# Performance work log

Measured on AMD Instinct MI355X. Metric: run time of the kernel, lower is better.

Reference implementation:

```python
import jax, jax.numpy as jnp
import numpy as np

B, T, C, NH = 4, 2048, 1024, 16
HD = C // NH  # head dim = 64


def setup_inputs() -> dict:
    key = jax.random.key(0)
    k1, k2, k3 = jax.random.split(key, 3)
    x = jax.random.normal(k1, (B, T, C), dtype=jnp.float32)
    w_attn = jax.random.normal(k2, (C, 3 * C), dtype=jnp.float32) * (1.0 / np.sqrt(C))
    b_attn = jnp.zeros((3 * C,), dtype=jnp.float32)
    w_proj = jax.random.normal(k3, (C, C), dtype=jnp.float32) * (1.0 / np.sqrt(C))
    b_proj = jnp.zeros((C,), dtype=jnp.float32)
    return {"x": x, "w_attn": w_attn, "b_attn": b_attn, "w_proj": w_proj, "b_proj": b_proj}


def reference(x, w_attn, b_attn, w_proj, b_proj):
    Bx, Tx, Cx = x.shape
    # fused QKV projection
    qkv = x @ w_attn + b_attn              # [B, T, 3C]
    q, k, v = jnp.split(qkv, 3, axis=-1)   # each [B, T, C]
    # split heads: [B, NH, T, HD]
    q = q.reshape(Bx, Tx, NH, HD).transpose(0, 2, 1, 3)
    k = k.reshape(Bx, Tx, NH, HD).transpose(0, 2, 1, 3)
    v = v.reshape(Bx, Tx, NH, HD).transpose(0, 2, 1, 3)
    scale = 1.0 / np.sqrt(HD)
    att = jnp.einsum('bhqd,bhkd->bhqk', q, k) * scale  # [B, NH, T, T]
    causal = jnp.tril(jnp.ones((Tx, Tx), dtype=bool))
    att = jnp.where(causal[None, None], att, -jnp.inf)
    att = jax.nn.softmax(att, axis=-1)
    y = jnp.einsum('bhqk,bhkd->bhqd', att, v)           # [B, NH, T, HD]
    y = y.transpose(0, 2, 1, 3).reshape(Bx, Tx, Cx)
    return y @ w_proj + b_proj
```

## Files before the change

kernel.cpp:

```cpp
#include <hip/hip_runtime.h>
#include <hip/hip_bf16.h>

#define B_SZ 4
#define T_SZ 2048
#define C_SZ 1024
#define NH_SZ 16
#define HD_SZ 64
#define M_SZ (B_SZ * T_SZ)

typedef __bf16 bf16x8 __attribute__((ext_vector_type(8)));
typedef __bf16 bf16x4 __attribute__((ext_vector_type(4)));
typedef float f32x4 __attribute__((ext_vector_type(4)));

__device__ __forceinline__ void async_ld16(__hip_bfloat16* lds, const __hip_bfloat16* g) {
  __builtin_amdgcn_global_load_lds(
      (const __attribute__((address_space(1))) void*)g,
      (__attribute__((address_space(3))) void*)lds, 16, 0, 0);
}

__device__ __forceinline__ void bar() {
  asm volatile("" ::: "memory");
  __builtin_amdgcn_s_barrier();
  asm volatile("" ::: "memory");
}

__device__ __forceinline__ bf16x8 frag32(const __hip_bfloat16* base, int row, int q) {
  const int byte = (row << 6) + (((q ^ (row >> 1)) & 3) << 4);
  return *(const bf16x8*)((const char*)base + byte);
}

__device__ __forceinline__ uint32_t pk2(float lo, float hi) {
  uint32_t r;
  asm("v_cvt_pk_bf16_f32 %0, %1, %2" : "=v"(r) : "v"(lo), "v"(hi));
  return r;
}

__global__ __launch_bounds__(256) void conv_bf16_kernel(
    const float* __restrict__ X, __hip_bfloat16* __restrict__ Y) {
  const int i = (blockIdx.x * 256 + threadIdx.x) * 4;
  float4 v = *(const float4*)&X[i];
  union { bf16x4 v; __hip_bfloat16 h[4]; } o;
  o.h[0] = __float2bfloat16(v.x); o.h[1] = __float2bfloat16(v.y);
  o.h[2] = __float2bfloat16(v.z); o.h[3] = __float2bfloat16(v.w);
  *(bf16x4*)&Y[i] = o.v;
}

template <int KD, int ND>
__global__ __launch_bounds__(256) void transpose_conv_kernel(
    const float* __restrict__ W, __hip_bfloat16* __restrict__ Wt) {
  __shared__ float sT[32][33];
  const int n0 = blockIdx.x * 32, k0 = blockIdx.y * 32;
  const int tid = threadIdx.x;
  {
    const int r = tid >> 3, c = (tid & 7) * 4;
    float4 v = *(const float4*)&W[(size_t)(k0 + r) * ND + n0 + c];
    sT[r][c] = v.x; sT[r][c + 1] = v.y; sT[r][c + 2] = v.z; sT[r][c + 3] = v.w;
  }
  __syncthreads();
  {
    const int n = tid >> 3, kq = (tid & 7) * 4;
    union { bf16x4 v; __hip_bfloat16 h[4]; } o;
#pragma unroll
    for (int j = 0; j < 4; ++j) o.h[j] = __float2bfloat16(sT[kq + j][n]);
    *(bf16x4*)&Wt[(size_t)(n0 + n) * KD + k0 + kq] = o.v;
  }
}


#define Q_PRESCALE 0.18033688011112042f

__global__ __launch_bounds__(512, 2) void gemm_tri256_qk(
    const __hip_bfloat16* __restrict__ A, const __hip_bfloat16* __restrict__ Bt,
    const float* __restrict__ bias,
    __hip_bfloat16* __restrict__ qR, __hip_bfloat16* __restrict__ kR) {
  __shared__ __align__(16) __hip_bfloat16 sA[3][256 * 32];
  __shared__ __align__(16) __hip_bfloat16 sB[3][256 * 32];

  const int tid = threadIdx.x;
  const int wave = tid >> 6, lane = tid & 63;
  const int quad = lane >> 4, l16 = lane & 15;
  const int wm = wave >> 2, wn = wave & 3;

  const int xcd = (int)blockIdx.x & 7, lb = (int)blockIdx.x >> 3;
  const int bm = (xcd * 4 + (lb >> 3)) * 256;
  const int bn = (lb & 7) * 256;

  const int srow = tid >> 2;
  const int scol = 8 * ((tid & 3) ^ ((tid >> 3) & 3));
  const int sdst = tid * 8;
  const __hip_bfloat16* gA = A + (size_t)(bm + srow) * C_SZ + scol;
  const __hip_bfloat16* gB = Bt + (size_t)(bn + srow) * C_SZ + scol;

  f32x4 acc[8][4];
#pragma unroll
  for (int m = 0; m < 8; ++m)
#pragma unroll
    for (int n = 0; n < 4; ++n) acc[m][n] = (f32x4){0.f, 0.f, 0.f, 0.f};

#define STG256(buf, kt)                                                         \
  do {                                                                          \
    async_ld16(&sA[buf][sdst], gA + (kt) * 32);                                 \
    async_ld16(&sA[buf][4096 + sdst], gA + (size_t)128 * C_SZ + (kt) * 32);     \
    async_ld16(&sB[buf][sdst], gB + (kt) * 32);                                 \
    async_ld16(&sB[buf][4096 + sdst], gB + (size_t)128 * C_SZ + (kt) * 32);     \
  } while (0)

  STG256(0, 0);
  STG256(1, 1);
  asm volatile("s_waitcnt vmcnt(4)" ::: "memory");
  bar();

  constexpr int NT = C_SZ / 32;
  int cur = 0;
  for (int kt = 0; kt < NT; ++kt) {
    const int stg = cur == 0 ? 2 : cur - 1;
    if (kt + 2 < NT) STG256(stg, kt + 2);

    const __hip_bfloat16* ab = sA[cur];
    const __hip_bfloat16* bb = sB[cur];
    bf16x8 af[8], bfr[4];
#pragma unroll
    for (int mq = 0; mq < 8; ++mq) af[mq] = frag32(ab, wm * 128 + mq * 16 + l16, quad);
#pragma unroll
    for (int nq = 0; nq < 4; ++nq) bfr[nq] = frag32(bb, wn * 64 + nq * 16 + l16, quad);
#pragma unroll
    for (int mq = 0; mq < 8; ++mq)
#pragma unroll
      for (int nq = 0; nq < 4; ++nq)
        acc[mq][nq] = __builtin_amdgcn_mfma_f32_16x16x32_bf16(af[mq], bfr[nq], acc[mq][nq], 0, 0, 0);

    if (kt + 1 < NT) {
      if (kt + 2 < NT) asm volatile("s_waitcnt vmcnt(4)" ::: "memory");
      else             asm volatile("s_waitcnt vmcnt(0)" ::: "memory");
      bar();
    }
    cur = cur == 2 ? 0 : cur + 1;
  }
#undef STG256

  float bv[4];
#pragma unroll
  for (int nq = 0; nq < 4; ++nq) bv[nq] = bias[bn + wn * 64 + nq * 16 + l16];
  const bool isQ = bn < C_SZ;
#pragma unroll
  for (int mq = 0; mq < 8; ++mq)
#pragma unroll
    for (int nq = 0; nq < 4; ++nq) {
      const int col = bn + wn * 64 + nq * 16 + l16;
      const int hh = (col >> 6) & 15, d = col & 63;
#pragma unroll
      for (int r = 0; r < 4; ++r) {
        const int row = bm + wm * 128 + mq * 16 + quad * 4 + r;
        const int bb_ = row >> 11, t = row & 2047;
        const size_t idx = ((size_t)(bb_ * 16 + hh) * T_SZ + t) * HD_SZ + d;
        const float val = acc[mq][nq][r] + bv[nq];
        if (isQ) qR[idx] = __float2bfloat16(val * Q_PRESCALE);
        else     kR[idx] = __float2bfloat16(val);
      }
    }
}

template <int MODE>
__global__ __launch_bounds__(256, 3) void gemm_tri128(
    const __hip_bfloat16* __restrict__ A, const __hip_bfloat16* __restrict__ Bt,
    const float* __restrict__ bias, float* __restrict__ Cf,
    __hip_bfloat16* __restrict__ vT) {
  __shared__ __align__(16) __hip_bfloat16 sA[3][128 * 32];
  __shared__ __align__(16) __hip_bfloat16 sB[3][128 * 32];

  const int tid = threadIdx.x;
  const int wave = tid >> 6, lane = tid & 63;
  const int quad = lane >> 4, l16 = lane & 15;
  const int rw = (wave & 1) * 64, cw = (wave >> 1) * 64;

  const int xcd = (int)blockIdx.x & 7, lb = (int)blockIdx.x >> 3;
  const int bm = (xcd * 8 + (lb >> 3)) * 128;
  const int bn = (lb & 7) * 128;

  const int srow = tid >> 2;
  const int scol = 8 * ((tid & 3) ^ ((tid >> 3) & 3));
  const int sdst = tid * 8;
  const __hip_bfloat16* gA = A + (size_t)(bm + srow) * C_SZ + scol;
  const __hip_bfloat16* gB = Bt + (size_t)(bn + srow) * C_SZ + scol;

  f32x4 acc[4][4];
#pragma unroll
  for (int i = 0; i < 4; ++i)
#pragma unroll
    for (int j = 0; j < 4; ++j) acc[i][j] = (f32x4){0.f, 0.f, 0.f, 0.f};

#define STG128(buf, kt)                                                        \
  do {                                                                         \
    async_ld16(&sA[buf][sdst], gA + (kt) * 32);                                \
    async_ld16(&sA[buf][2048 + sdst], gA + (size_t)64 * C_SZ + (kt) * 32);     \
    async_ld16(&sB[buf][sdst], gB + (kt) * 32);                                \
    async_ld16(&sB[buf][2048 + sdst], gB + (size_t)64 * C_SZ + (kt) * 32);     \
  } while (0)

  STG128(0, 0);
  STG128(1, 1);
  asm volatile("s_waitcnt vmcnt(4)" ::: "memory");
  bar();

  constexpr int NT = C_SZ / 32;
  int cur = 0;
  for (int kt = 0; kt < NT; ++kt) {
    const int stg = cur == 0 ? 2 : cur - 1;
    if (kt + 2 < NT) STG128(stg, kt + 2);

    const __hip_bfloat16* ab = sA[cur];
    const __hip_bfloat16* bb = sB[cur];
    bf16x8 af[4], bfr[4];
#pragma unroll
    for (int mq = 0; mq < 4; ++mq) af[mq] = frag32(ab, rw + mq * 16 + l16, quad);
#pragma unroll
    for (int nq = 0; nq < 4; ++nq) bfr[nq] = frag32(bb, cw + nq * 16 + l16, quad);
#pragma unroll
    for (int mq = 0; mq < 4; ++mq)
#pragma unroll
      for (int nq = 0; nq < 4; ++nq)
        acc[mq][nq] = __builtin_amdgcn_mfma_f32_16x16x32_bf16(af[mq], bfr[nq], acc[mq][nq], 0, 0, 0);

    if (kt + 1 < NT) {
      if (kt + 2 < NT) asm volatile("s_waitcnt vmcnt(4)" ::: "memory");
      else             asm volatile("s_waitcnt vmcnt(0)" ::: "memory");
      bar();
    }
    cur = cur == 2 ? 0 : cur + 1;
  }
#undef STG128

  float bv[4];
#pragma unroll
  for (int nq = 0; nq < 4; ++nq) bv[nq] = bias[bn + cw + nq * 16 + l16];
#pragma unroll
  for (int mq = 0; mq < 4; ++mq)
#pragma unroll
    for (int nq = 0; nq < 4; ++nq) {
      const int col = bn + cw + nq * 16 + l16;
#pragma unroll
      for (int r = 0; r < 4; ++r) {
        const int row = bm + rw + mq * 16 + quad * 4 + r;
        const float val = acc[mq][nq][r] + bv[nq];
        if (MODE == 0) {
          const int bb_ = row >> 11, t = row & 2047;
          const int hh = col >> 6, d = col & 63;
          vT[((size_t)(bb_ * 16 + hh) * HD_SZ + d) * T_SZ + t] = __float2bfloat16(val);
        } else {
          Cf[(size_t)row * C_SZ + col] = val;
        }
      }
    }
}

#define ATT_ST 72

__global__ __launch_bounds__(256, 5) void attn_mfma_kernel(
    const __hip_bfloat16* __restrict__ qR, const __hip_bfloat16* __restrict__ kR,
    const __hip_bfloat16* __restrict__ vT, __hip_bfloat16* __restrict__ y) {
  __shared__ __align__(16) __hip_bfloat16 sQ[64][ATT_ST];
  __shared__ __align__(16) __hip_bfloat16 sK[64][ATT_ST];
  __shared__ __align__(16) __hip_bfloat16 sVt[64][ATT_ST];

  const int bh = blockIdx.x;
  const int tile = (int)gridDim.y - 1 - blockIdx.y;
  const int t0 = tile * 64;
  const int tid = threadIdx.x;
  const int wave = tid >> 6, lane = tid & 63;
  const int quad = lane >> 4, l16 = lane & 15;
  const int wrow0 = wave * 16;

  const __hip_bfloat16* qb = qR + (size_t)bh * T_SZ * HD_SZ;
  const __hip_bfloat16* kb = kR + (size_t)bh * T_SZ * HD_SZ;
  const __hip_bfloat16* vb = vT + (size_t)bh * HD_SZ * T_SZ;

  const int sr = tid >> 2, sc = (tid & 3) * 16;

  const bool uSel = (quad & 1) != 0;
  const bool cSel = (quad >> 1) != 0;
  const int srcE = l16 + 32 * (quad & 1) + 16 * (quad >> 1);
  const int srcO = srcE ^ 16;

  {
    const __hip_bfloat16* src = qb + (size_t)t0 * HD_SZ + tid * 16;
    *(float4*)&sQ[sr][sc] = *(const float4*)src;
    *(float4*)&sQ[sr][sc + 8] = *(const float4*)(src + 8);
  }

  float4 krg0, krg1, vrg0, vrg1;
  {
    const __hip_bfloat16* ks = kb + tid * 16;
    krg0 = *(const float4*)ks;
    krg1 = *(const float4*)(ks + 8);
    const __hip_bfloat16* vs = vb + (size_t)sr * T_SZ + sc;
    vrg0 = *(const float4*)vs;
    vrg1 = *(const float4*)(vs + 8);
  }

  __syncthreads();
  bf16x8 qa0 = *(const bf16x8*)&sQ[wrow0 + l16][quad * 8];
  bf16x8 qa1 = *(const bf16x8*)&sQ[wrow0 + l16][32 + quad * 8];

  float lacc = 0.f;
  f32x4 o[4];
#pragma unroll
  for (int nn = 0; nn < 4; ++nn) o[nn] = (f32x4){0.f, 0.f, 0.f, 0.f};

  for (int j0 = 0; j0 <= t0; j0 += 64) {
    *(float4*)&sK[sr][sc] = krg0;
    *(float4*)&sK[sr][sc + 8] = krg1;
    *(float4*)&sVt[sr][sc] = vrg0;
    *(float4*)&sVt[sr][sc + 8] = vrg1;
    if (j0 + 64 <= t0) {
      const __hip_bfloat16* ks = kb + (size_t)(j0 + 64) * HD_SZ + tid * 16;
      krg0 = *(const float4*)ks;
      krg1 = *(const float4*)(ks + 8);
      const __hip_bfloat16* vs = vb + (size_t)sr * T_SZ + j0 + 64 + sc;
      vrg0 = *(const float4*)vs;
      vrg1 = *(const float4*)(vs + 8);
    }
    __syncthreads();

    f32x4 s[4];
    __builtin_amdgcn_s_setprio(1);
#pragma unroll
    for (int sub = 0; sub < 4; ++sub) {
      s[sub] = (f32x4){0.f, 0.f, 0.f, 0.f};
      bf16x8 kf0 = *(const bf16x8*)&sK[sub * 16 + l16][quad * 8];
      s[sub] = __builtin_amdgcn_mfma_f32_16x16x32_bf16(kf0, qa0, s[sub], 0, 0, 0);
      bf16x8 kf1 = *(const bf16x8*)&sK[sub * 16 + l16][32 + quad * 8];
      s[sub] = __builtin_amdgcn_mfma_f32_16x16x32_bf16(kf1, qa1, s[sub], 0, 0, 0);
    }
    __builtin_amdgcn_s_setprio(0);

    if (j0 == t0) {
      const int qrow = wrow0 + l16;
#pragma unroll
      for (int sub = 0; sub < 4; ++sub)
#pragma unroll
        for (int r = 0; r < 4; ++r)
          if (sub * 16 + quad * 4 + r > qrow) s[sub][r] = -1e30f;
    }

#pragma unroll
    for (int sub = 0; sub < 4; ++sub)
#pragma unroll
      for (int r = 0; r < 4; ++r) s[sub][r] = __builtin_amdgcn_exp2f(s[sub][r]);
#pragma unroll
    for (int sub = 0; sub < 4; ++sub)
      lacc += (s[sub][0] + s[sub][1]) + (s[sub][2] + s[sub][3]);

    uint32_t pk[4][2];
#pragma unroll
    for (int sub = 0; sub < 4; ++sub)
#pragma unroll
      for (int h = 0; h < 2; ++h)
        pk[sub][h] = pk2(s[sub][2 * h], s[sub][2 * h + 1]);

    uint32_t g0 = (uint32_t)__shfl((int)(uSel ? pk[1][0] : pk[0][0]), srcE, 64);
    uint32_t g1 = (uint32_t)__shfl((int)(uSel ? pk[0][0] : pk[1][0]), srcO, 64);
    uint32_t g2 = (uint32_t)__shfl((int)(uSel ? pk[3][0] : pk[2][0]), srcE, 64);
    uint32_t g3 = (uint32_t)__shfl((int)(uSel ? pk[2][0] : pk[3][0]), srcO, 64);
    uint32_t g4 = (uint32_t)__shfl((int)(uSel ? pk[1][1] : pk[0][1]), srcE, 64);
    uint32_t g5 = (uint32_t)__shfl((int)(uSel ? pk[0][1] : pk[1][1]), srcO, 64);
    uint32_t g6 = (uint32_t)__shfl((int)(uSel ? pk[3][1] : pk[2][1]), srcE, 64);
    uint32_t g7 = (uint32_t)__shfl((int)(uSel ? pk[2][1] : pk[3][1]), srcO, 64);

    union PU { uint32_t d[4]; bf16x8 v; };
    PU A0, A1;
    A0.d[0] = cSel ? g1 : g0;  A0.d[1] = cSel ? g5 : g4;
    A0.d[2] = cSel ? g0 : g1;  A0.d[3] = cSel ? g4 : g5;
    A1.d[0] = cSel ? g3 : g2;  A1.d[1] = cSel ? g7 : g6;
    A1.d[2] = cSel ? g2 : g3;  A1.d[3] = cSel ? g6 : g7;

    __builtin_amdgcn_s_setprio(1);
#pragma unroll
    for (int nn = 0; nn < 4; ++nn) {
      bf16x8 vf0 = *(const bf16x8*)&sVt[nn * 16 + l16][quad * 8];
      o[nn] = __builtin_amdgcn_mfma_f32_16x16x32_bf16(A0.v, vf0, o[nn], 0, 0, 0);
      bf16x8 vf1 = *(const bf16x8*)&sVt[nn * 16 + l16][32 + quad * 8];
      o[nn] = __builtin_amdgcn_mfma_f32_16x16x32_bf16(A1.v, vf1, o[nn], 0, 0, 0);
    }
    __builtin_amdgcn_s_setprio(0);

    if (j0 < t0) __syncthreads();
  }

  lacc += __shfl_xor(lacc, 16);
  lacc += __shfl_xor(lacc, 32);
  float inv[4];
#pragma unroll
  for (int r = 0; r < 4; ++r)
    inv[r] = 1.0f / __shfl(lacc, (lane & 48) + quad * 4 + r, 64);

  const int b = bh >> 4, h = bh & 15;
#pragma unroll
  for (int nn = 0; nn < 4; ++nn)
#pragma unroll
    for (int r = 0; r < 4; ++r) {
      const int t = t0 + wrow0 + quad * 4 + r;
      y[((size_t)b * T_SZ + t) * C_SZ + h * HD_SZ + nn * 16 + l16] =
          __float2bfloat16(o[nn][r] * inv[r]);
    }
}

extern "C" void kernel_launch(void* const* d_in, const int* in_sizes, int n_in,
                              void* d_out, int out_size, void* d_ws, size_t ws_size,
                              hipStream_t stream) {
  const float* x      = (const float*)d_in[0];
  const float* w_attn = (const float*)d_in[1];
  const float* b_attn = (const float*)d_in[2];
  const float* w_proj = (const float*)d_in[3];
  const float* b_proj = (const float*)d_in[4];
  float* out = (float*)d_out;

  __hip_bfloat16* xb  = (__hip_bfloat16*)d_ws;
  __hip_bfloat16* waT = xb + (size_t)M_SZ * C_SZ;
  __hip_bfloat16* wpT = waT + (size_t)3 * C_SZ * C_SZ;
  __hip_bfloat16* qR  = wpT + (size_t)C_SZ * C_SZ;
  __hip_bfloat16* kR  = qR + (size_t)M_SZ * C_SZ;
  __hip_bfloat16* vT  = kR + (size_t)M_SZ * C_SZ;
  __hip_bfloat16* yb  = xb;

  conv_bf16_kernel<<<(M_SZ * C_SZ) / (256 * 4), 256, 0, stream>>>(x, xb);
  transpose_conv_kernel<C_SZ, 3 * C_SZ><<<dim3(96, 32), 256, 0, stream>>>(w_attn, waT);
  transpose_conv_kernel<C_SZ, C_SZ><<<dim3(32, 32), 256, 0, stream>>>(w_proj, wpT);

  gemm_tri256_qk<<<dim3(256), 512, 0, stream>>>(xb, waT, b_attn, qR, kR);

  gemm_tri128<0><<<dim3(512), 256, 0, stream>>>(
      xb, waT + (size_t)2 * C_SZ * C_SZ, b_attn + 2 * C_SZ, nullptr, vT);

  attn_mfma_kernel<<<dim3(B_SZ * NH_SZ, T_SZ / 64), 256, 0, stream>>>(qR, kR, vT, yb);

  gemm_tri128<1><<<dim3(512), 256, 0, stream>>>(
      (const __hip_bfloat16*)yb, wpT, b_proj, out, nullptr);
}
```

Before: 259.8 us.

## Process 128 query rows per attention block to reuse K/V tiles

Each attention block now handles 128 query rows instead of 64, with every wave owning two 16-row groups that share the same K and V^T fragments loaded from LDS. This halves the K/V global-to-LDS traffic and barriers per query row. The causal mask becomes a general per-row comparison over the extra diagonal tile. The cost is more registers (launch bounds lowered from 5 to 3), half as many blocks (1024), and coarser causal load balance.

```diff
diff --git a/kernel.cpp b/kernel.cpp
--- a/kernel.cpp
+++ b/kernel.cpp
@@ -255,20 +255,47 @@
 
 #define ATT_ST 72
 
-__global__ __launch_bounds__(256, 5) void attn_mfma_kernel(
+__device__ __forceinline__ void p_exchange(
+    const f32x4& s0, const f32x4& s1, const f32x4& s2, const f32x4& s3,
+    bool uSel, bool cSel, int srcE, int srcO, bf16x8& A0v, bf16x8& A1v) {
+  uint32_t pk[4][2];
+  pk[0][0] = pk2(s0[0], s0[1]); pk[0][1] = pk2(s0[2], s0[3]);
+  pk[1][0] = pk2(s1[0], s1[1]); pk[1][1] = pk2(s1[2], s1[3]);
+  pk[2][0] = pk2(s2[0], s2[1]); pk[2][1] = pk2(s2[2], s2[3]);
+  pk[3][0] = pk2(s3[0], s3[1]); pk[3][1] = pk2(s3[2], s3[3]);
+
+  uint32_t g0 = (uint32_t)__shfl((int)(uSel ? pk[1][0] : pk[0][0]), srcE, 64);
+  uint32_t g1 = (uint32_t)__shfl((int)(uSel ? pk[0][0] : pk[1][0]), srcO, 64);
+  uint32_t g2 = (uint32_t)__shfl((int)(uSel ? pk[3][0] : pk[2][0]), srcE, 64);
+  uint32_t g3 = (uint32_t)__shfl((int)(uSel ? pk[2][0] : pk[3][0]), srcO, 64);
+  uint32_t g4 = (uint32_t)__shfl((int)(uSel ? pk[1][1] : pk[0][1]), srcE, 64);
+  uint32_t g5 = (uint32_t)__shfl((int)(uSel ? pk[0][1] : pk[1][1]), srcO, 64);
+  uint32_t g6 = (uint32_t)__shfl((int)(uSel ? pk[3][1] : pk[2][1]), srcE, 64);
+  uint32_t g7 = (uint32_t)__shfl((int)(uSel ? pk[2][1] : pk[3][1]), srcO, 64);
+
+  union PU { uint32_t d[4]; bf16x8 v; } A0, A1;
+  A0.d[0] = cSel ? g1 : g0;  A0.d[1] = cSel ? g5 : g4;
+  A0.d[2] = cSel ? g0 : g1;  A0.d[3] = cSel ? g4 : g5;
+  A1.d[0] = cSel ? g3 : g2;  A1.d[1] = cSel ? g7 : g6;
+  A1.d[2] = cSel ? g2 : g3;  A1.d[3] = cSel ? g6 : g7;
+  A0v = A0.v;
+  A1v = A1.v;
+}
+
+__global__ __launch_bounds__(256, 3) void attn_mfma_kernel(
     const __hip_bfloat16* __restrict__ qR, const __hip_bfloat16* __restrict__ kR,
     const __hip_bfloat16* __restrict__ vT, __hip_bfloat16* __restrict__ y) {
-  __shared__ __align__(16) __hip_bfloat16 sQ[64][ATT_ST];
+  __shared__ __align__(16) __hip_bfloat16 sQ[128][ATT_ST];
   __shared__ __align__(16) __hip_bfloat16 sK[64][ATT_ST];
   __shared__ __align__(16) __hip_bfloat16 sVt[64][ATT_ST];
 
   const int bh = blockIdx.x;
   const int tile = (int)gridDim.y - 1 - blockIdx.y;
-  const int t0 = tile * 64;
+  const int t0 = tile * 128;
   const int tid = threadIdx.x;
   const int wave = tid >> 6, lane = tid & 63;
   const int quad = lane >> 4, l16 = lane & 15;
-  const int wrow0 = wave * 16;
+  const int wrowQ = wave * 32;
 
   const __hip_bfloat16* qb = qR + (size_t)bh * T_SZ * HD_SZ;
   const __hip_bfloat16* kb = kR + (size_t)bh * T_SZ * HD_SZ;
@@ -285,6 +312,9 @@
     const __hip_bfloat16* src = qb + (size_t)t0 * HD_SZ + tid * 16;
     *(float4*)&sQ[sr][sc] = *(const float4*)src;
     *(float4*)&sQ[sr][sc + 8] = *(const float4*)(src + 8);
+    const __hip_bfloat16* src2 = src + 64 * HD_SZ;
+    *(float4*)&sQ[64 + sr][sc] = *(const float4*)src2;
+    *(float4*)&sQ[64 + sr][sc + 8] = *(const float4*)(src2 + 8);
   }
 
   float4 krg0, krg1, vrg0, vrg1;
@@ -298,20 +328,27 @@
   }
 
   __syncthreads();
-  bf16x8 qa0 = *(const bf16x8*)&sQ[wrow0 + l16][quad * 8];
-  bf16x8 qa1 = *(const bf16x8*)&sQ[wrow0 + l16][32 + quad * 8];
-
-  float lacc = 0.f;
-  f32x4 o[4];
-#pragma unroll
-  for (int nn = 0; nn < 4; ++nn) o[nn] = (f32x4){0.f, 0.f, 0.f, 0.f};
-
-  for (int j0 = 0; j0 <= t0; j0 += 64) {
+  bf16x8 qa[2][2];
+#pragma unroll
+  for (int g = 0; g < 2; ++g) {
+    qa[g][0] = *(const bf16x8*)&sQ[wrowQ + g * 16 + l16][quad * 8];
+    qa[g][1] = *(const bf16x8*)&sQ[wrowQ + g * 16 + l16][32 + quad * 8];
+  }
+
+  float lacc0 = 0.f, lacc1 = 0.f;
+  f32x4 o[2][4];
+#pragma unroll
+  for (int g = 0; g < 2; ++g)
+#pragma unroll
+    for (int nn = 0; nn < 4; ++nn) o[g][nn] = (f32x4){0.f, 0.f, 0.f, 0.f};
+
+  const int jmax = t0 + 64;
+  for (int j0 = 0; j0 <= jmax; j0 += 64) {
     *(float4*)&sK[sr][sc] = krg0;
     *(float4*)&sK[sr][sc + 8] = krg1;
     *(float4*)&sVt[sr][sc] = vrg0;
     *(float4*)&sVt[sr][sc + 8] = vrg1;
-    if (j0 + 64 <= t0) {
+    if (j0 + 64 <= jmax) {
       const __hip_bfloat16* ks = kb + (size_t)(j0 + 64) * HD_SZ + tid * 16;
       krg0 = *(const float4*)ks;
       krg1 = *(const float4*)(ks + 8);
@@ -321,87 +358,96 @@
     }
     __syncthreads();
 
-    f32x4 s[4];
+    f32x4 s0[4], s1[4];
     __builtin_amdgcn_s_setprio(1);
 #pragma unroll
     for (int sub = 0; sub < 4; ++sub) {
-      s[sub] = (f32x4){0.f, 0.f, 0.f, 0.f};
       bf16x8 kf0 = *(const bf16x8*)&sK[sub * 16 + l16][quad * 8];
-      s[sub] = __builtin_amdgcn_mfma_f32_16x16x32_bf16(kf0, qa0, s[sub], 0, 0, 0);
       bf16x8 kf1 = *(const bf16x8*)&sK[sub * 16 + l16][32 + quad * 8];
-      s[sub] = __builtin_amdgcn_mfma_f32_16x16x32_bf16(kf1, qa1, s[sub], 0, 0, 0);
+      s0[sub] = (f32x4){0.f, 0.f, 0.f, 0.f};
+      s0[sub] = __builtin_amdgcn_mfma_f32_16x16x32_bf16(kf0, qa[0][0], s0[sub], 0, 0, 0);
+      s0[sub] = __builtin_amdgcn_mfma_f32_16x16x32_bf16(kf1, qa[0][1], s0[sub], 0, 0, 0);
+      s1[sub] = (f32x4){0.f, 0.f, 0.f, 0.f};
+      s1[sub] = __builtin_amdgcn_mfma_f32_16x16x32_bf16(kf0, qa[1][0], s1[sub], 0, 0, 0);
+      s1[sub] = __builtin_amdgcn_mfma_f32_16x16x32_bf16(kf1, qa[1][1], s1[sub], 0, 0, 0);
     }
     __builtin_amdgcn_s_setprio(0);
 
-    if (j0 == t0) {
-      const int qrow = wrow0 + l16;
-#pragma unroll
-      for (int sub = 0; sub < 4; ++sub)
-#pragma unroll
-        for (int r = 0; r < 4; ++r)
-          if (sub * 16 + quad * 4 + r > qrow) s[sub][r] = -1e30f;
+    {
+      const int qb0 = t0 + wrowQ;
+      if (j0 + 63 > qb0) {
+        const int qrow = qb0 + l16;
+#pragma unroll
+        for (int sub = 0; sub < 4; ++sub)
+#pragma unroll
+          for (int r = 0; r < 4; ++r)
+            if (j0 + sub * 16 + quad * 4 + r > qrow) s0[sub][r] = -1e30f;
+      }
+      const int qb1 = qb0 + 16;
+      if (j0 + 63 > qb1) {
+        const int qrow = qb1 + l16;
+#pragma unroll
+        for (int sub = 0; sub < 4; ++sub)
+#pragma unroll
+          for (int r = 0; r < 4; ++r)
+            if (j0 + sub * 16 + quad * 4 + r > qrow) s1[sub][r] = -1e30f;
+      }
     }
 
 #pragma unroll
     for (int sub = 0; sub < 4; ++sub)
 #pragma unroll
-      for (int r = 0; r < 4; ++r) s[sub][r] = __builtin_amdgcn_exp2f(s[sub][r]);
-#pragma unroll
-    for (int sub = 0; sub < 4; ++sub)
-      lacc += (s[sub][0] + s[sub][1]) + (s[sub][2] + s[sub][3]);
-
-    uint32_t pk[4][2];
-#pragma unroll
-    for (int sub = 0; sub < 4; ++sub)
-#pragma unroll
-      for (int h = 0; h < 2; ++h)
-        pk[sub][h] = pk2(s[sub][2 * h], s[sub][2 * h + 1]);
-
-    uint32_t g0 = (uint32_t)__shfl((int)(uSel ? pk[1][0] : pk[0][0]), srcE, 64);
-    uint32_t g1 = (uint32_t)__shfl((int)(uSel ? pk[0][0] : pk[1][0]), srcO, 64);
-    uint32_t g2 = (uint32_t)__shfl((int)(uSel ? pk[3][0] : pk[2][0]), srcE, 64);
-    uint32_t g3 = (uint32_t)__shfl((int)(uSel ? pk[2][0] : pk[3][0]), srcO, 64);
-    uint32_t g4 = (uint32_t)__shfl((int)(uSel ? pk[1][1] : pk[0][1]), srcE, 64);
-    uint32_t g5 = (uint32_t)__shfl((int)(uSel ? pk[0][1] : pk[1][1]), srcO, 64);
-    uint32_t g6 = (uint32_t)__shfl((int)(uSel ? pk[3][1] : pk[2][1]), srcE, 64);
-    uint32_t g7 = (uint32_t)__shfl((int)(uSel ? pk[2][1] : pk[3][1]), srcO, 64);
-
-    union PU { uint32_t d[4]; bf16x8 v; };
-    PU A0, A1;
-    A0.d[0] = cSel ? g1 : g0;  A0.d[1] = cSel ? g5 : g4;
-    A0.d[2] = cSel ? g0 : g1;  A0.d[3] = cSel ? g4 : g5;
-    A1.d[0] = cSel ? g3 : g2;  A1.d[1] = cSel ? g7 : g6;
-    A1.d[2] = cSel ? g2 : g3;  A1.d[3] = cSel ? g6 : g7;
+      for (int r = 0; r < 4; ++r) {
+        s0[sub][r] = __builtin_amdgcn_exp2f(s0[sub][r]);
+        s1[sub][r] = __builtin_amdgcn_exp2f(s1[sub][r]);
+      }
+#pragma unroll
+    for (int sub = 0; sub < 4; ++sub) {
+      lacc0 += (s0[sub][0] + s0[sub][1]) + (s0[sub][2] + s0[sub][3]);
+      lacc1 += (s1[sub][0] + s1[sub][1]) + (s1[sub][2] + s1[sub][3]);
+    }
+
+    bf16x8 A0g0, A1g0, A0g1, A1g1;
+    p_exchange(s0[0], s0[1], s0[2], s0[3], uSel, cSel, srcE, srcO, A0g0, A1g0);
+    p_exchange(s1[0], s1[1], s1[2], s1[3], uSel, cSel, srcE, srcO, A0g1, A1g1);
 
     __builtin_amdgcn_s_setprio(1);
 #pragma unroll
     for (int nn = 0; nn < 4; ++nn) {
       bf16x8 vf0 = *(const bf16x8*)&sVt[nn * 16 + l16][quad * 8];
-      o[nn] = __builtin_amdgcn_mfma_f32_16x16x32_bf16(A0.v, vf0, o[nn], 0, 0, 0);
       bf16x8 vf1 = *(const bf16x8*)&sVt[nn * 16 + l16][32 + quad * 8];
-      o[nn] = __builtin_amdgcn_mfma_f32_16x16x32_bf16(A1.v, vf1, o[nn], 0, 0, 0);
+      o[0][nn] = __builtin_amdgcn_mfma_f32_16x16x32_bf16(A0g0, vf0, o[0][nn], 0, 0, 0);
+      o[0][nn] = __builtin_amdgcn_mfma_f32_16x16x32_bf16(A1g0, vf1, o[0][nn], 0, 0, 0);
+      o[1][nn] = __builtin_amdgcn_mfma_f32_16x16x32_bf16(A0g1, vf0, o[1][nn], 0, 0, 0);
+      o[1][nn] = __builtin_amdgcn_mfma_f32_16x16x32_bf16(A1g1, vf1, o[1][nn], 0, 0, 0);
     }
     __builtin_amdgcn_s_setprio(0);
 
-    if (j0 < t0) __syncthreads();
-  }
-
-  lacc += __shfl_xor(lacc, 16);
-  lacc += __shfl_xor(lacc, 32);
-  float inv[4];
-#pragma unroll
-  for (int r = 0; r < 4; ++r)
-    inv[r] = 1.0f / __shfl(lacc, (lane & 48) + quad * 4 + r, 64);
+    if (j0 < jmax) __syncthreads();
+  }
+
+  lacc0 += __shfl_xor(lacc0, 16);
+  lacc0 += __shfl_xor(lacc0, 32);
+  lacc1 += __shfl_xor(lacc1, 16);
+  lacc1 += __shfl_xor(lacc1, 32);
+  float inv[2][4];
+#pragma unroll
+  for (int r = 0; r < 4; ++r) {
+    inv[0][r] = 1.0f / __shfl(lacc0, (lane & 48) + quad * 4 + r, 64);
+    inv[1][r] = 1.0f / __shfl(lacc1, (lane & 48) + quad * 4 + r, 64);
+  }
 
   const int b = bh >> 4, h = bh & 15;
 #pragma unroll
-  for (int nn = 0; nn < 4; ++nn)
-#pragma unroll
-    for (int r = 0; r < 4; ++r) {
-      const int t = t0 + wrow0 + quad * 4 + r;
-      y[((size_t)b * T_SZ + t) * C_SZ + h * HD_SZ + nn * 16 + l16] =
-          __float2bfloat16(o[nn][r] * inv[r]);
-    }
+  for (int g = 0; g < 2; ++g)
+#pragma unroll
+    for (int nn = 0; nn < 4; ++nn)
+#pragma unroll
+      for (int r = 0; r < 4; ++r) {
+        const int t = t0 + wrowQ + g * 16 + quad * 4 + r;
+        y[((size_t)b * T_SZ + t) * C_SZ + h * HD_SZ + nn * 16 + l16] =
+            __float2bfloat16(o[g][nn][r] * inv[g][r]);
+      }
 }
 
 extern "C" void kernel_launch(void* const* d_in, const int* in_sizes, int n_in,
@@ -431,7 +477,7 @@
   gemm_tri128<0><<<dim3(512), 256, 0, stream>>>(
       xb, waT + (size_t)2 * C_SZ * C_SZ, b_attn + 2 * C_SZ, nullptr, vT);
 
-  attn_mfma_kernel<<<dim3(B_SZ * NH_SZ, T_SZ / 64), 256, 0, stream>>>(qR, kR, vT, yb);
+  attn_mfma_kernel<<<dim3(B_SZ * NH_SZ, T_SZ / 128), 256, 0, stream>>>(qR, kR, vT, yb);
 
   gemm_tri128<1><<<dim3(512), 256, 0, stream>>>(
       (const __hip_bfloat16*)yb, wpT, b_proj, out, nullptr);
```

Result: faster. 249.8 us (-3.8%).
